# Performance work log

Hardware: AMD Instinct MI355X
Metric: run time of the kernel (lower is better)

## Reference

```python
import jax, jax.numpy as jnp
import numpy as np

VOCAB = 32000
EMB = 256
UNITS = 1024


def setup_inputs() -> dict:
    key = jax.random.key(0)
    ks = jax.random.split(key, 6)
    B, S = 128, 256
    x = jax.random.randint(ks[0], (B, S), 0, VOCAB, dtype=jnp.int32)
    hidden = jnp.zeros((B, UNITS), jnp.float32)
    # Parameters (Keras GRU v2, reset_after=True): kernel W [EMB, 3*UNITS],
    # recurrent kernel U [UNITS, 3*UNITS], bias b [2, 3*UNITS] (input bias, recurrent bias)
    emb = jax.random.normal(ks[1], (VOCAB, EMB), jnp.float32) * 0.05
    W = jax.random.normal(ks[2], (EMB, 3 * UNITS), jnp.float32) * (1.0 / np.sqrt(EMB))
    U = jax.random.normal(ks[3], (UNITS, 3 * UNITS), jnp.float32) * (1.0 / np.sqrt(UNITS))
    b = jnp.zeros((2, 3 * UNITS), jnp.float32)
    return {"x": x, "hidden": hidden, "emb": emb, "W": W, "U": U, "b": b}


def _gru_seq(xp, hidden, U, b_rec):
    # xp: [S, B, 3H] precomputed input projections (incl. input bias)
    H = hidden.shape[-1]

    def step(h, xt):
        rec = h @ U + b_rec                       # [B, 3H]
        xz, xr, xh = xt[:, :H], xt[:, H:2 * H], xt[:, 2 * H:]
        rz, rr, rh = rec[:, :H], rec[:, H:2 * H], rec[:, 2 * H:]
        z = jax.nn.sigmoid(xz + rz)
        r = jax.nn.sigmoid(xr + rr)
        hh = jnp.tanh(xh + r * rh)                # reset_after=True
        h_new = z * h + (1.0 - z) * hh
        return h_new, h_new

    state, outs = jax.lax.scan(step, hidden, xp)
    return outs, state


def reference(x, hidden, emb, W, U, b):
    xe = emb[x]                                   # [B, S, EMB]
    # Precompute all input-side projections in one big GEMM
    xp = jnp.einsum('bse,eh->bsh', xe, W) + b[0]  # [B, S, 3H]
    xp = jnp.swapaxes(xp, 0, 1)                   # [S, B, 3H]
    outs, state = _gru_seq(xp, hidden, U, b[1])
    output = jnp.swapaxes(outs, 0, 1)             # [B, S, H]
    return output, state
```

## Files before the change

kernel.cpp:

```cpp
#include <hip/hip_runtime.h>

#define B_   128
#define S_   256
#define EMB_ 256
#define H_   1024
#define NH3  3072

#define G_      8
#define NW      32
#define MG      16
#define HS      32
#define THREADS 768

typedef _Float16 f16;
typedef _Float16 h8 __attribute__((ext_vector_type(8)));
typedef float    f4 __attribute__((ext_vector_type(4)));
typedef unsigned long long u64;

#define AL64(pp) __hip_atomic_load((pp), __ATOMIC_RELAXED, __HIP_MEMORY_SCOPE_AGENT)
#define ALI(pp)  __hip_atomic_load((pp), __ATOMIC_RELAXED, __HIP_MEMORY_SCOPE_AGENT)

__global__ void gather_kernel(const int* __restrict__ x, const float* __restrict__ emb,
                              f16* __restrict__ xe16) {
  int m = blockIdx.x, k = threadIdx.x;
  int b = m & 127, s = m >> 7;
  int row = x[b * S_ + s];
  xe16[m * EMB_ + k] = (f16)emb[row * EMB_ + k];
}

__global__ void transpose_cvt(const float* __restrict__ in, f16* __restrict__ out,
                              int K, int N) {
  __shared__ float tile[32][33];
  int n0 = blockIdx.x * 32, k0 = blockIdx.y * 32;
  int tx = threadIdx.x & 31, ty = threadIdx.x >> 5;
#pragma unroll
  for (int i = 0; i < 4; ++i)
    tile[ty + 8 * i][tx] = in[(k0 + ty + 8 * i) * N + n0 + tx];
  __syncthreads();
#pragma unroll
  for (int i = 0; i < 4; ++i)
    out[(n0 + ty + 8 * i) * K + k0 + tx] = (f16)tile[tx][ty + 8 * i];
}

__launch_bounds__(THREADS, 3)
__global__ void gru_kernel(const f16* __restrict__ xe16, const f16* __restrict__ Ut,
                           const f16* __restrict__ Wt, const float* __restrict__ hidden,
                           const float* __restrict__ bvec, float* __restrict__ out,
                           f16* __restrict__ h16, int* __restrict__ flags) {
  __shared__ f16   h_lds[MG * H_];
  __shared__ f16   xe_lds[2][MG * EMB_];
  __shared__ float recS[4][MG][100];
  __shared__ float recU[4][MG][36];

  const int tid = threadIdx.x;
  const int bid = blockIdx.x;
  const int g   = bid & 7;
  const int w   = bid >> 3;
  const int gb0 = g * MG;
  const int hc0 = w * HS;

  const int lane = tid & 63;
  const int wv   = tid >> 6;
  const int ksp  = wv & 3;
  const int cp   = wv >> 2;
  const int ln   = lane & 15;
  const int klo  = lane >> 4;
  const int bl   = tid >> 5;
  const int jl   = tid & 31;

  int* gflags = flags + g * NW;

  h8 uf0[8], uf1[8], wf0[2], wf1[2];
  {
    const f16* u0 = Ut + (size_t)(cp * H_ + hc0 + ln) * H_ + ksp * 256 + klo * 8;
    const f16* u1 = u0 + (size_t)16 * H_;
#pragma unroll
    for (int kt = 0; kt < 8; ++kt) { uf0[kt] = *(const h8*)(u0 + kt * 32);
                                     uf1[kt] = *(const h8*)(u1 + kt * 32); }
    const f16* w0 = Wt + (size_t)(cp * H_ + hc0 + ln) * EMB_ + ksp * 64 + klo * 8;
    const f16* w1 = w0 + 16 * EMB_;
#pragma unroll
    for (int kt = 0; kt < 2; ++kt) { wf0[kt] = *(const h8*)(w0 + kt * 32);
                                     wf1[kt] = *(const h8*)(w1 + kt * 32); }
  }
#pragma unroll
  for (int kt = 0; kt < 8; ++kt) { asm volatile("" : "+v"(uf0[kt])); asm volatile("" : "+v"(uf1[kt])); }
  asm volatile("" : "+v"(wf0[0]), "+v"(wf0[1]), "+v"(wf1[0]), "+v"(wf1[1]));

  float hprev = 0.f, bz = 0.f, brr = 0.f, bxh = 0.f, brh = 0.f;
  size_t obase = 0, soff = 0;
  if (tid < 512) {
    int col = hc0 + jl;
    bz  = bvec[col] + bvec[NH3 + col];
    brr = bvec[H_ + col] + bvec[NH3 + H_ + col];
    bxh = bvec[2 * H_ + col];
    brh = bvec[NH3 + 2 * H_ + col];
    hprev = hidden[(size_t)(gb0 + bl) * H_ + col];
    obase = ((size_t)(gb0 + bl) * S_) * H_ + col;
    soff  = (size_t)(gb0 + bl) * H_ + col;
  }

  for (int idx = tid; idx < MG * H_ / 4; idx += THREADS) {
    int r = idx >> 8, c4 = idx & 255;
    float4 hv = ((const float4*)(hidden + (size_t)(gb0 + r) * H_))[c4];
    unsigned lo = ((unsigned)__builtin_bit_cast(unsigned short, (f16)hv.y) << 16)
                |  (unsigned)__builtin_bit_cast(unsigned short, (f16)hv.x);
    unsigned hi = ((unsigned)__builtin_bit_cast(unsigned short, (f16)hv.w) << 16)
                |  (unsigned)__builtin_bit_cast(unsigned short, (f16)hv.z);
    uint2 pk = {lo, hi};
    *(uint2*)((char*)h_lds + r * 2048 + ((c4 * 8) ^ ((r & 7) << 4))) = pk;
  }
  for (int idx = tid; idx < MG * EMB_ / 8; idx += THREADS) {
    uint4 v = ((const uint4*)(xe16 + (size_t)gb0 * EMB_))[idx];
    int r = idx >> 5, c = idx & 31;
    *(uint4*)((char*)xe_lds[0] + r * 512 + ((c * 16) ^ ((r & 7) << 4))) = v;
  }
  __syncthreads();

  const int s0p = wv, s1p = wv + 12, s2p = wv + 24;
  const int pr  = lane >> 2;
  const int pc  = (lane & 3) * 2;

  for (int t = 0; t < S_; ++t) {
    f4 a0 = {0.f,0.f,0.f,0.f}, a1 = {0.f,0.f,0.f,0.f};
    f4 a2 = {0.f,0.f,0.f,0.f}, a3 = {0.f,0.f,0.f,0.f};
    const char* hb = (const char*)h_lds + ln * 2048;
    const char* xb = (const char*)xe_lds[t & 1] + ln * 512;
    const int rm = (ln & 7) << 4;
#pragma unroll
    for (int kt = 0; kt < 8; ++kt) {
      h8 a = *(const h8*)(hb + ((ksp * 512 + kt * 64 + klo * 16) ^ rm));
      a0 = __builtin_amdgcn_mfma_f32_16x16x32_f16(a, uf0[kt], a0, 0, 0, 0);
      a1 = __builtin_amdgcn_mfma_f32_16x16x32_f16(a, uf1[kt], a1, 0, 0, 0);
    }
#pragma unroll
    for (int kt = 0; kt < 2; ++kt) {
      h8 a = *(const h8*)(xb + ((ksp * 128 + kt * 64 + klo * 16) ^ rm));
      a2 = __builtin_amdgcn_mfma_f32_16x16x32_f16(a, wf0[kt], a2, 0, 0, 0);
      a3 = __builtin_amdgcn_mfma_f32_16x16x32_f16(a, wf1[kt], a3, 0, 0, 0);
    }
#pragma unroll
    for (int j = 0; j < 4; ++j) {
      int r = klo * 4 + j;
      if (cp < 2) {
        recS[ksp][r][cp * 32 + ln]      = a0[j] + a2[j];
        recS[ksp][r][cp * 32 + 16 + ln] = a1[j] + a3[j];
      } else {
        recS[ksp][r][64 + ln] = a2[j];
        recS[ksp][r][80 + ln] = a3[j];
        recU[ksp][r][ln]      = a0[j];
        recU[ksp][r][16 + ln] = a1[j];
      }
    }
    __syncthreads();

    float outv = 0.f;
    if (tid < 512) {
      float az = recS[0][bl][jl] + recS[1][bl][jl] + recS[2][bl][jl] + recS[3][bl][jl] + bz;
      float ar = recS[0][bl][32+jl] + recS[1][bl][32+jl] + recS[2][bl][32+jl] + recS[3][bl][32+jl] + brr;
      float xh = recS[0][bl][64+jl] + recS[1][bl][64+jl] + recS[2][bl][64+jl] + recS[3][bl][64+jl] + bxh;
      float rhu = recU[0][bl][jl] + recU[1][bl][jl] + recU[2][bl][jl] + recU[3][bl][jl] + brh;
      float z  = 1.f / (1.f + __expf(-az));
      float r  = 1.f / (1.f + __expf(-ar));
      float hh = 1.f - 2.f / (1.f + __expf(2.f * (xh + r * rhu)));
      float hn = z * hprev + (1.f - z) * hh;
      hprev = hn; outv = hn;
      if (t < S_ - 1) {
        unsigned short hb16 = __builtin_bit_cast(unsigned short, (f16)hn);
        __hip_atomic_store((unsigned short*)(h16 + (size_t)((t + 1) & 1) * (B_ * H_)) + soff,
                           hb16, __ATOMIC_RELAXED, __HIP_MEMORY_SCOPE_AGENT);
      }
    }
    if (t == S_ - 1) {
      if (tid < 512) {
        out[obase + (size_t)t * H_] = outv;
        out[(size_t)B_ * S_ * H_ + soff] = outv;
      }
      break;
    }

    asm volatile("s_waitcnt vmcnt(0)" ::: "memory");
    __syncthreads();
    if (tid == 0)
      __hip_atomic_store(&gflags[w], t + 1, __ATOMIC_RELAXED, __HIP_MEMORY_SCOPE_AGENT);

    if (tid < 512) {
      out[obase + (size_t)t * H_] = outv;
    } else {
      const uint4* src = (const uint4*)(xe16 + ((size_t)(t + 1) * B_ + gb0) * EMB_);
      char* dst = (char*)xe_lds[(t + 1) & 1];
#pragma unroll
      for (int i = 0; i < 2; ++i) {
        int idx = (tid - 512) * 2 + i;
        uint4 v = src[idx];
        int r = idx >> 5, c = idx & 31;
        *(uint4*)(dst + r * 512 + ((c * 16) ^ ((r & 7) << 4))) = v;
      }
    }

    {
      const int need = t + 1;
      const u64* hbuf = (const u64*)(h16 + (size_t)((t + 1) & 1) * (B_ * H_));
      const int rowu = (gb0 + pr) * 256;
      for (;;) { int f = ALI(&gflags[s0p]); if (f >= need) break; __builtin_amdgcn_s_sleep(1); }
      for (;;) { int f = ALI(&gflags[s1p]); if (f >= need) break; __builtin_amdgcn_s_sleep(1); }
      if (wv < 8)
        for (;;) { int f = ALI(&gflags[s2p]); if (f >= need) break; __builtin_amdgcn_s_sleep(1); }
      u64 va0 = AL64(hbuf + rowu + s0p * 8 + pc);
      u64 va1 = AL64(hbuf + rowu + s0p * 8 + pc + 1);
      u64 vb0 = AL64(hbuf + rowu + s1p * 8 + pc);
      u64 vb1 = AL64(hbuf + rowu + s1p * 8 + pc + 1);
      u64 vc0 = 0, vc1 = 0;
      if (wv < 8) {
        vc0 = AL64(hbuf + rowu + s2p * 8 + pc);
        vc1 = AL64(hbuf + rowu + s2p * 8 + pc + 1);
      }
      char* hd = (char*)h_lds + pr * 2048;
      const int prm = (pr & 7) << 4;
      *(u64*)(hd + ((s0p * 64 + pc * 8    ) ^ prm)) = va0;
      *(u64*)(hd + ((s0p * 64 + pc * 8 + 8) ^ prm)) = va1;
      *(u64*)(hd + ((s1p * 64 + pc * 8    ) ^ prm)) = vb0;
      *(u64*)(hd + ((s1p * 64 + pc * 8 + 8) ^ prm)) = vb1;
      if (wv < 8) {
        *(u64*)(hd + ((s2p * 64 + pc * 8    ) ^ prm)) = vc0;
        *(u64*)(hd + ((s2p * 64 + pc * 8 + 8) ^ prm)) = vc1;
      }
    }
    __syncthreads();
  }
}

extern "C" void kernel_launch(void* const* d_in, const int* in_sizes, int n_in,
                              void* d_out, int out_size, void* d_ws, size_t ws_size,
                              hipStream_t stream) {
  const int*   x      = (const int*)  d_in[0];
  const float* hidden = (const float*)d_in[1];
  const float* emb    = (const float*)d_in[2];
  const float* W      = (const float*)d_in[3];
  const float* U      = (const float*)d_in[4];
  const float* bvec   = (const float*)d_in[5];
  float* out = (float*)d_out;

  char* ws = (char*)d_ws;
  f16* Ut    = (f16*)(ws);
  f16* Wt    = (f16*)(ws + 6291456);
  f16* xe16  = (f16*)(ws + 7864320);
  f16* h16   = (f16*)(ws + 24641536);
  int* flags = (int*)(ws + 25165824);

  hipMemsetAsync(flags, 0, 1024, stream);
  hipLaunchKernelGGL(transpose_cvt, dim3(NH3 / 32, H_ / 32), dim3(256), 0, stream,
                     U, Ut, H_, NH3);
  hipLaunchKernelGGL(transpose_cvt, dim3(NH3 / 32, EMB_ / 32), dim3(256), 0, stream,
                     W, Wt, EMB_, NH3);
  hipLaunchKernelGGL(gather_kernel, dim3(B_ * S_), dim3(EMB_), 0, stream, x, emb, xe16);

  void* args[] = { (void*)&xe16, (void*)&Ut, (void*)&Wt, (void*)&hidden,
                   (void*)&bvec, (void*)&out, (void*)&h16, (void*)&flags };
  hipLaunchCooperativeKernel(reinterpret_cast<void*>(gru_kernel),
                             dim3(G_ * NW), dim3(THREADS), args, 0, stream);
}
```

Before: 1.064 ms.

## Feed recurrent MFMA A-operands directly from global h instead of LDS staging

Removes the shared-memory copy of the full hidden state. Each wave now waits only on the flags of the 8 producer blocks covering its K-slice, using a wave-wide vote, then loads its fp16 h fragments straight from global memory into MFMA operands. At t=0 it reads and converts the fp32 initial hidden state directly. This drops the LDS staging writes and lets each wave start its matmul as soon as its own slice is ready rather than after a full block barrier. In exchange, every wave issues redundant global loads on the critical path, and the launch bound drops to 2 blocks per CU.

```diff
diff --git a/kernel.cpp b/kernel.cpp
--- a/kernel.cpp
+++ b/kernel.cpp
@@ -16,6 +16,7 @@
 typedef _Float16 h8 __attribute__((ext_vector_type(8)));
 typedef float    f4 __attribute__((ext_vector_type(4)));
 typedef unsigned long long u64;
+typedef u64 u64x2 __attribute__((ext_vector_type(2)));
 
 #define AL64(pp) __hip_atomic_load((pp), __ATOMIC_RELAXED, __HIP_MEMORY_SCOPE_AGENT)
 #define ALI(pp)  __hip_atomic_load((pp), __ATOMIC_RELAXED, __HIP_MEMORY_SCOPE_AGENT)
@@ -42,12 +43,11 @@
     out[(n0 + ty + 8 * i) * K + k0 + tx] = (f16)tile[tx][ty + 8 * i];
 }
 
-__launch_bounds__(THREADS, 3)
+__launch_bounds__(THREADS, 2)
 __global__ void gru_kernel(const f16* __restrict__ xe16, const f16* __restrict__ Ut,
                            const f16* __restrict__ Wt, const float* __restrict__ hidden,
                            const float* __restrict__ bvec, float* __restrict__ out,
                            f16* __restrict__ h16, int* __restrict__ flags) {
-  __shared__ f16   h_lds[MG * H_];
   __shared__ f16   xe_lds[2][MG * EMB_];
   __shared__ float recS[4][MG][100];
   __shared__ float recU[4][MG][36];
@@ -100,16 +100,6 @@
     soff  = (size_t)(gb0 + bl) * H_ + col;
   }
 
-  for (int idx = tid; idx < MG * H_ / 4; idx += THREADS) {
-    int r = idx >> 8, c4 = idx & 255;
-    float4 hv = ((const float4*)(hidden + (size_t)(gb0 + r) * H_))[c4];
-    unsigned lo = ((unsigned)__builtin_bit_cast(unsigned short, (f16)hv.y) << 16)
-                |  (unsigned)__builtin_bit_cast(unsigned short, (f16)hv.x);
-    unsigned hi = ((unsigned)__builtin_bit_cast(unsigned short, (f16)hv.w) << 16)
-                |  (unsigned)__builtin_bit_cast(unsigned short, (f16)hv.z);
-    uint2 pk = {lo, hi};
-    *(uint2*)((char*)h_lds + r * 2048 + ((c4 * 8) ^ ((r & 7) << 4))) = pk;
-  }
   for (int idx = tid; idx < MG * EMB_ / 8; idx += THREADS) {
     uint4 v = ((const uint4*)(xe16 + (size_t)gb0 * EMB_))[idx];
     int r = idx >> 5, c = idx & 31;
@@ -117,28 +107,55 @@
   }
   __syncthreads();
 
-  const int s0p = wv, s1p = wv + 12, s2p = wv + 24;
-  const int pr  = lane >> 2;
-  const int pc  = (lane & 3) * 2;
+  const int rowelem = (gb0 + (lane & 15)) * H_ + (lane >> 4) * 8;
 
   for (int t = 0; t < S_; ++t) {
     f4 a0 = {0.f,0.f,0.f,0.f}, a1 = {0.f,0.f,0.f,0.f};
     f4 a2 = {0.f,0.f,0.f,0.f}, a3 = {0.f,0.f,0.f,0.f};
-    const char* hb = (const char*)h_lds + ln * 2048;
-    const char* xb = (const char*)xe_lds[t & 1] + ln * 512;
-    const int rm = (ln & 7) << 4;
-#pragma unroll
-    for (int kt = 0; kt < 8; ++kt) {
-      h8 a = *(const h8*)(hb + ((ksp * 512 + kt * 64 + klo * 16) ^ rm));
-      a0 = __builtin_amdgcn_mfma_f32_16x16x32_f16(a, uf0[kt], a0, 0, 0, 0);
-      a1 = __builtin_amdgcn_mfma_f32_16x16x32_f16(a, uf1[kt], a1, 0, 0, 0);
-    }
-#pragma unroll
-    for (int kt = 0; kt < 2; ++kt) {
-      h8 a = *(const h8*)(xb + ((ksp * 128 + kt * 64 + klo * 16) ^ rm));
-      a2 = __builtin_amdgcn_mfma_f32_16x16x32_f16(a, wf0[kt], a2, 0, 0, 0);
-      a3 = __builtin_amdgcn_mfma_f32_16x16x32_f16(a, wf1[kt], a3, 0, 0, 0);
-    }
+    {
+      const char* xb = (const char*)xe_lds[t & 1] + ln * 512;
+      const int rm = (ln & 7) << 4;
+#pragma unroll
+      for (int kt = 0; kt < 2; ++kt) {
+        h8 a = *(const h8*)(xb + ((ksp * 128 + kt * 64 + klo * 16) ^ rm));
+        a2 = __builtin_amdgcn_mfma_f32_16x16x32_f16(a, wf0[kt], a2, 0, 0, 0);
+        a3 = __builtin_amdgcn_mfma_f32_16x16x32_f16(a, wf1[kt], a3, 0, 0, 0);
+      }
+    }
+
+    if (t == 0) {
+      const float* hrow = hidden + rowelem;
+#pragma unroll
+      for (int kt = 0; kt < 8; ++kt) {
+        const float4* q = (const float4*)(hrow + (ksp * 8 + kt) * 32);
+        float4 qa = q[0], qb = q[1];
+        h8 a;
+        a[0] = (f16)qa.x; a[1] = (f16)qa.y; a[2] = (f16)qa.z; a[3] = (f16)qa.w;
+        a[4] = (f16)qb.x; a[5] = (f16)qb.y; a[6] = (f16)qb.z; a[7] = (f16)qb.w;
+        a0 = __builtin_amdgcn_mfma_f32_16x16x32_f16(a, uf0[kt], a0, 0, 0, 0);
+        a1 = __builtin_amdgcn_mfma_f32_16x16x32_f16(a, uf1[kt], a1, 0, 0, 0);
+      }
+    } else {
+      {
+        int f = 0x7fffffff;
+        for (;;) {
+          if (lane < 8) f = ALI(&gflags[ksp * 8 + lane]);
+          if (__all(f >= t)) break;
+          __builtin_amdgcn_s_sleep(1);
+        }
+      }
+      const u64* hb64 = (const u64*)(h16 + (size_t)(t & 1) * (B_ * H_));
+#pragma unroll
+      for (int kt = 0; kt < 8; ++kt) {
+        const u64* p = hb64 + ((rowelem + (ksp * 8 + kt) * 32) >> 2);
+        u64 d0 = AL64(p), d1 = AL64(p + 1);
+        u64x2 dv = {d0, d1};
+        h8 a = __builtin_bit_cast(h8, dv);
+        a0 = __builtin_amdgcn_mfma_f32_16x16x32_f16(a, uf0[kt], a0, 0, 0, 0);
+        a1 = __builtin_amdgcn_mfma_f32_16x16x32_f16(a, uf1[kt], a1, 0, 0, 0);
+      }
+    }
+
 #pragma unroll
     for (int j = 0; j < 4; ++j) {
       int r = klo * 4 + j;
@@ -197,35 +214,6 @@
         *(uint4*)(dst + r * 512 + ((c * 16) ^ ((r & 7) << 4))) = v;
       }
     }
-
-    {
-      const int need = t + 1;
-      const u64* hbuf = (const u64*)(h16 + (size_t)((t + 1) & 1) * (B_ * H_));
-      const int rowu = (gb0 + pr) * 256;
-      for (;;) { int f = ALI(&gflags[s0p]); if (f >= need) break; __builtin_amdgcn_s_sleep(1); }
-      for (;;) { int f = ALI(&gflags[s1p]); if (f >= need) break; __builtin_amdgcn_s_sleep(1); }
-      if (wv < 8)
-        for (;;) { int f = ALI(&gflags[s2p]); if (f >= need) break; __builtin_amdgcn_s_sleep(1); }
-      u64 va0 = AL64(hbuf + rowu + s0p * 8 + pc);
-      u64 va1 = AL64(hbuf + rowu + s0p * 8 + pc + 1);
-      u64 vb0 = AL64(hbuf + rowu + s1p * 8 + pc);
-      u64 vb1 = AL64(hbuf + rowu + s1p * 8 + pc + 1);
-      u64 vc0 = 0, vc1 = 0;
-      if (wv < 8) {
-        vc0 = AL64(hbuf + rowu + s2p * 8 + pc);
-        vc1 = AL64(hbuf + rowu + s2p * 8 + pc + 1);
-      }
-      char* hd = (char*)h_lds + pr * 2048;
-      const int prm = (pr & 7) << 4;
-      *(u64*)(hd + ((s0p * 64 + pc * 8    ) ^ prm)) = va0;
-      *(u64*)(hd + ((s0p * 64 + pc * 8 + 8) ^ prm)) = va1;
-      *(u64*)(hd + ((s1p * 64 + pc * 8    ) ^ prm)) = vb0;
-      *(u64*)(hd + ((s1p * 64 + pc * 8 + 8) ^ prm)) = vb1;
-      if (wv < 8) {
-        *(u64*)(hd + ((s2p * 64 + pc * 8    ) ^ prm)) = vc0;
-        *(u64*)(hd + ((s2p * 64 + pc * 8 + 8) ^ prm)) = vc1;
-      }
-    }
     __syncthreads();
   }
 }
```

After: 1.904 ms. 79.0% more time.
